# Performance work log

Hardware: AMD Instinct MI355X
Metric: run time of the kernel (lower is better)

The kernel has to match this reference:

```python
import jax, jax.numpy as jnp
import numpy as np

NUM_HEAD = 8
D_MODEL = 512
HEAD_DIM = D_MODEL // NUM_HEAD
SCALING = HEAD_DIM ** (-0.5)
B, NQ, NK = 2, 2048, 2048


def setup_inputs() -> dict:
    key = jax.random.key(0)
    ks = jax.random.split(key, 12)
    s = 1.0 / np.sqrt(D_MODEL)
    return {
        "q": jax.random.normal(ks[0], (B, NQ, D_MODEL), jnp.float32),
        "k": jax.random.normal(ks[1], (B, NK, D_MODEL), jnp.float32),
        "v": jax.random.normal(ks[2], (B, NK, D_MODEL), jnp.float32),
        "mask_head": jax.random.uniform(ks[3], (B, NUM_HEAD, NQ, NK), jnp.float32),
        "pearson_matrix": jax.random.normal(ks[4], (B, NUM_HEAD, NK, NK), jnp.float32),
        "Wq": jax.random.uniform(ks[5], (D_MODEL, D_MODEL), jnp.float32, -s, s),
        "bq": jax.random.uniform(ks[6], (D_MODEL,), jnp.float32, -s, s),
        "Wk": jax.random.uniform(ks[7], (D_MODEL, D_MODEL), jnp.float32, -s, s),
        "bk": jax.random.uniform(ks[8], (D_MODEL,), jnp.float32, -s, s),
        "Wv": jax.random.uniform(ks[9], (D_MODEL, D_MODEL), jnp.float32, -s, s),
        "bv": jax.random.uniform(ks[10], (D_MODEL,), jnp.float32, -s, s),
    }


def _split_heads(x):
    b, n, _ = x.shape
    return x.reshape(b, n, NUM_HEAD, HEAD_DIM).transpose(0, 2, 1, 3)  # b h n d


def reference(q, k, v, mask_head, pearson_matrix, Wq, bq, Wk, bk, Wv, bv):
    queries = _split_heads(q @ Wq.T + bq)
    keys = _split_heads(k @ Wk.T + bk)
    values = _split_heads(v @ Wv.T + bv)
    energy = jnp.einsum('bhqd,bhkd->bhqk', queries, keys) * SCALING
    att = jax.nn.softmax(energy, axis=-1)
    att = att * mask_head
    # einsum 'bhqk,bhkk->bhqk' = multiply by diagonal of pearson over last two axes
    diag = jnp.diagonal(pearson_matrix, axis1=-2, axis2=-1)  # b h k
    att = att * diag[:, :, None, :]
    agg = jnp.einsum('bhqk,bhkd->bhqd', att, values)
    b, h, n, d = agg.shape
    return agg.transpose(0, 2, 1, 3).reshape(b, n, h * d)
```

## Files before the change

kernel.cpp:

```cpp
#include <hip/hip_runtime.h>

#define NUM_HEAD 8
#define D_MODEL  512
#define HEAD_DIM 64
#define NSEQ     2048
#define SCALE_LOG2E 0.18033688011112042f

typedef __attribute__((ext_vector_type(8))) short bf16x8;
typedef __attribute__((ext_vector_type(4))) float f32x4;

static __device__ __forceinline__ unsigned short f2bf(float f) {
    unsigned u = __builtin_bit_cast(unsigned, f);
    u += 0x7fffu + ((u >> 16) & 1u);
    return (unsigned short)(u >> 16);
}
static __device__ __forceinline__ float bf2f(unsigned short h) {
    unsigned u = ((unsigned)h) << 16;
    return __builtin_bit_cast(float, u);
}
static __device__ __forceinline__ unsigned pk2(float a, float b) {
    return (unsigned)f2bf(a) | ((unsigned)f2bf(b) << 16);
}

#define PSTR 40

__global__ __launch_bounds__(256) void proj_kernel(
    const float* __restrict__ X, const float* __restrict__ W,
    const float* __restrict__ bias, unsigned short* __restrict__ outp)
{
    __shared__ unsigned short lA[128 * PSTR];
    __shared__ unsigned short lB[64 * PSTR];

    const int tid  = threadIdx.x;
    const int lane = tid & 63, wid = tid >> 6;
    const int quad = lane >> 4, l15 = lane & 15;
    const int wm = (wid >> 1) * 64;
    const int wn = (wid & 1) * 32;
    const int m0 = blockIdx.x * 128, n0 = blockIdx.y * 64;

    f32x4 acc[4][2];
    const f32x4 zf = {0.f, 0.f, 0.f, 0.f};
#pragma unroll
    for (int mi = 0; mi < 4; mi++)
#pragma unroll
        for (int ni = 0; ni < 2; ni++) acc[mi][ni] = zf;

    const int arow = tid >> 1, akc = (tid & 1) * 16;
    const int brow = tid >> 2, bkc = (tid & 3) * 8;

    for (int k0 = 0; k0 < D_MODEL; k0 += 32) {
        const float* ap = X + (m0 + arow) * D_MODEL + k0 + akc;
        float4 a0 = *(const float4*)(ap);
        float4 a1 = *(const float4*)(ap + 4);
        float4 a2 = *(const float4*)(ap + 8);
        float4 a3 = *(const float4*)(ap + 12);
        uint4 w0, w1;
        w0.x = pk2(a0.x, a0.y); w0.y = pk2(a0.z, a0.w);
        w0.z = pk2(a1.x, a1.y); w0.w = pk2(a1.z, a1.w);
        w1.x = pk2(a2.x, a2.y); w1.y = pk2(a2.z, a2.w);
        w1.z = pk2(a3.x, a3.y); w1.w = pk2(a3.z, a3.w);
        *(uint4*)&lA[arow * PSTR + akc]     = w0;
        *(uint4*)&lA[arow * PSTR + akc + 8] = w1;
        const float* bp = W + (n0 + brow) * D_MODEL + k0 + bkc;
        float4 b0 = *(const float4*)(bp);
        float4 b1 = *(const float4*)(bp + 4);
        uint4 wb;
        wb.x = pk2(b0.x, b0.y); wb.y = pk2(b0.z, b0.w);
        wb.z = pk2(b1.x, b1.y); wb.w = pk2(b1.z, b1.w);
        *(uint4*)&lB[brow * PSTR + bkc] = wb;
        __syncthreads();

        bf16x8 aF[4], bF[2];
#pragma unroll
        for (int mi = 0; mi < 4; mi++)
            aF[mi] = *(const bf16x8*)&lA[(wm + mi * 16 + l15) * PSTR + quad * 8];
#pragma unroll
        for (int ni = 0; ni < 2; ni++)
            bF[ni] = *(const bf16x8*)&lB[(wn + ni * 16 + l15) * PSTR + quad * 8];
#pragma unroll
        for (int mi = 0; mi < 4; mi++)
#pragma unroll
            for (int ni = 0; ni < 2; ni++)
                acc[mi][ni] = __builtin_amdgcn_mfma_f32_16x16x32_bf16(
                    aF[mi], bF[ni], acc[mi][ni], 0, 0, 0);
        __syncthreads();
    }

    const float bv0 = bias[n0 + wn + l15];
    const float bv1 = bias[n0 + wn + 16 + l15];
#pragma unroll
    for (int mi = 0; mi < 4; mi++) {
        const int mbase = m0 + wm + mi * 16 + quad * 4;
#pragma unroll
        for (int ni = 0; ni < 2; ni++) {
            const int c = n0 + wn + ni * 16 + l15;
            const int h = c >> 6, d = c & 63;
            const float bb_add = ni ? bv1 : bv0;
#pragma unroll
            for (int r = 0; r < 4; r++) {
                const int mm = mbase + r;
                const int bb = mm >> 11, n = mm & 2047;
                const float val = acc[mi][ni][r] + bb_add;
                outp[((bb * NUM_HEAD + h) * NSEQ + n) * HEAD_DIM + d] = f2bf(val);
            }
        }
    }
}

__global__ void diag_kernel(const float* __restrict__ pearson,
                            float* __restrict__ diag)
{
    const int t = blockIdx.x * blockDim.x + threadIdx.x;
    const int bh = t >> 11, kk = t & 2047;
    diag[t] = pearson[((size_t)(bh * NSEQ + kk)) * NSEQ + kk];
}

#define VSTR 72

__global__ __launch_bounds__(256) void attn_kernel(
    const unsigned short* __restrict__ Qp, const unsigned short* __restrict__ Kp,
    const unsigned short* __restrict__ Vp, const float* __restrict__ diag,
    const float* __restrict__ mask, float* __restrict__ out)
{
    __shared__ unsigned short lVt[64 * VSTR];
    __shared__ unsigned short lP[64 * VSTR];

    const int tid  = threadIdx.x;
    const int lane = tid & 63, wid = tid >> 6;
    const int quad = lane >> 4, l15 = lane & 15;
    const int bh = blockIdx.y;
    const int q0 = blockIdx.x * 64;

    const unsigned short* Qb = Qp + (size_t)bh * NSEQ * HEAD_DIM;
    const unsigned short* Kb = Kp + (size_t)bh * NSEQ * HEAD_DIM;
    const unsigned short* Vb = Vp + (size_t)bh * NSEQ * HEAD_DIM;
    const float* maskb = mask + (size_t)bh * NSEQ * NSEQ + (size_t)q0 * NSEQ;
    const float* diagb = diag + bh * NSEQ;

    bf16x8 qF[2];
    {
        const unsigned short* qp = Qb + (q0 + wid * 16 + l15) * HEAD_DIM + quad * 8;
        qF[0] = *(const bf16x8*)qp;
        qF[1] = *(const bf16x8*)(qp + 32);
    }

    const f32x4 zf = {0.f, 0.f, 0.f, 0.f};
    f32x4 oacc[4] = {zf, zf, zf, zf};
    float lacc[4] = {0.f, 0.f, 0.f, 0.f};

    const int vrow = tid >> 2;
    const int vdb  = (tid & 3) * 16;

    for (int kt = 0; kt < NSEQ; kt += 64) {
        bf16x8 kF[4][2];
#pragma unroll
        for (int nt = 0; nt < 4; nt++) {
            const unsigned short* kp = Kb + (kt + nt * 16 + l15) * HEAD_DIM + quad * 8;
            kF[nt][0] = *(const bf16x8*)kp;
            kF[nt][1] = *(const bf16x8*)(kp + 32);
        }
        float mv[4][4];
#pragma unroll
        for (int cf = 0; cf < 4; cf++)
#pragma unroll
            for (int r = 0; r < 4; r++)
                mv[cf][r] = maskb[(size_t)(wid * 16 + quad * 4 + r) * NSEQ + kt + cf * 16 + l15];

        {
            const float dg = diagb[kt + vrow];
            const unsigned short* vp = Vb + (kt + vrow) * HEAD_DIM + vdb;
            union { uint4 u; unsigned short s[8]; } va, vb2;
            va.u  = *(const uint4*)vp;
            vb2.u = *(const uint4*)(vp + 8);
#pragma unroll
            for (int i = 0; i < 8; i++) {
                lVt[(vdb + i) * VSTR + vrow]     = f2bf(bf2f(va.s[i]) * dg);
                lVt[(vdb + 8 + i) * VSTR + vrow] = f2bf(bf2f(vb2.s[i]) * dg);
            }
        }

        f32x4 sacc[4];
#pragma unroll
        for (int nt = 0; nt < 4; nt++) {
            sacc[nt] = __builtin_amdgcn_mfma_f32_16x16x32_bf16(qF[0], kF[nt][0], zf, 0, 0, 0);
            sacc[nt] = __builtin_amdgcn_mfma_f32_16x16x32_bf16(qF[1], kF[nt][1], sacc[nt], 0, 0, 0);
        }

#pragma unroll
        for (int cf = 0; cf < 4; cf++) {
#pragma unroll
            for (int r = 0; r < 4; r++) {
                const float p = __builtin_amdgcn_exp2f(sacc[cf][r] * SCALE_LOG2E);
                lacc[r] += p;
                lP[(wid * 16 + quad * 4 + r) * VSTR + cf * 16 + l15] = f2bf(p * mv[cf][r]);
            }
        }
        __syncthreads();

#pragma unroll
        for (int ks = 0; ks < 2; ks++) {
            const bf16x8 aP = *(const bf16x8*)&lP[(wid * 16 + l15) * VSTR + ks * 32 + quad * 8];
#pragma unroll
            for (int nt = 0; nt < 4; nt++) {
                const bf16x8 bV = *(const bf16x8*)&lVt[(nt * 16 + l15) * VSTR + ks * 32 + quad * 8];
                oacc[nt] = __builtin_amdgcn_mfma_f32_16x16x32_bf16(aP, bV, oacc[nt], 0, 0, 0);
            }
        }
        __syncthreads();
    }

#pragma unroll
    for (int r = 0; r < 4; r++) {
        float v = lacc[r];
        v += __shfl_xor(v, 1);
        v += __shfl_xor(v, 2);
        v += __shfl_xor(v, 4);
        v += __shfl_xor(v, 8);
        lacc[r] = v;
    }

    const int b = bh >> 3, h = bh & 7;
#pragma unroll
    for (int nt = 0; nt < 4; nt++)
#pragma unroll
        for (int r = 0; r < 4; r++) {
            const int qrow = q0 + wid * 16 + quad * 4 + r;
            out[((size_t)b * NSEQ + qrow) * D_MODEL + h * HEAD_DIM + nt * 16 + l15] =
                oacc[nt][r] / lacc[r];
        }
}

extern "C" void kernel_launch(void* const* d_in, const int* in_sizes, int n_in,
                              void* d_out, int out_size, void* d_ws, size_t ws_size,
                              hipStream_t stream) {
    const float* q       = (const float*)d_in[0];
    const float* k       = (const float*)d_in[1];
    const float* v       = (const float*)d_in[2];
    const float* mask    = (const float*)d_in[3];
    const float* pearson = (const float*)d_in[4];
    const float* Wq      = (const float*)d_in[5];
    const float* bq      = (const float*)d_in[6];
    const float* Wk      = (const float*)d_in[7];
    const float* bk      = (const float*)d_in[8];
    const float* Wv      = (const float*)d_in[9];
    const float* bv      = (const float*)d_in[10];

    unsigned short* Qp = (unsigned short*)d_ws;
    unsigned short* Kp = Qp + 2097152;
    unsigned short* Vp = Kp + 2097152;
    float* diag = (float*)((char*)d_ws + 12582912);
    float* out = (float*)d_out;

    proj_kernel<<<dim3(32, 8), 256, 0, stream>>>(q, Wq, bq, Qp);
    proj_kernel<<<dim3(32, 8), 256, 0, stream>>>(k, Wk, bk, Kp);
    proj_kernel<<<dim3(32, 8), 256, 0, stream>>>(v, Wv, bv, Vp);
    diag_kernel<<<dim3(128), 256, 0, stream>>>(pearson, diag);
    attn_kernel<<<dim3(32, 16), 256, 0, stream>>>(Qp, Kp, Vp, diag, mask, out);
}
```

Measured before the change: 589.9 us.

## Pre-transpose V, fold diag into P, register double-buffer K/mask tiles

The projection kernel now runs Q, K and V in a single launch using blockIdx.z, and writes V transposed (head_dim x seq) with packed 4-wide stores. The attention kernel reads V fragments straight from global memory, so the LDS transpose of V and both block-wide __syncthreads are gone; each wave keeps a private P buffer. The pearson diagonal is applied to P instead of V. K, mask and diag for the next tile are prefetched into registers (ping-pong) while the current tile is computed. In exchange, register pressure rises and V is re-read from global/L2 by every wave.

```diff
diff --git a/kernel.cpp b/kernel.cpp
--- a/kernel.cpp
+++ b/kernel.cpp
@@ -25,11 +25,20 @@
 #define PSTR 40
 
 __global__ __launch_bounds__(256) void proj_kernel(
-    const float* __restrict__ X, const float* __restrict__ W,
-    const float* __restrict__ bias, unsigned short* __restrict__ outp)
+    const float* __restrict__ Xq, const float* __restrict__ Xk, const float* __restrict__ Xv,
+    const float* __restrict__ Wq, const float* __restrict__ Wk, const float* __restrict__ Wv,
+    const float* __restrict__ Bq, const float* __restrict__ Bk, const float* __restrict__ Bv,
+    unsigned short* __restrict__ Oq, unsigned short* __restrict__ Ok,
+    unsigned short* __restrict__ Ov)
 {
     __shared__ unsigned short lA[128 * PSTR];
     __shared__ unsigned short lB[64 * PSTR];
+
+    const int z = blockIdx.z;
+    const float* X    = (z == 0) ? Xq : (z == 1) ? Xk : Xv;
+    const float* W    = (z == 0) ? Wq : (z == 1) ? Wk : Wv;
+    const float* bias = (z == 0) ? Bq : (z == 1) ? Bk : Bv;
+    unsigned short* outp = (z == 0) ? Oq : (z == 1) ? Ok : Ov;
 
     const int tid  = threadIdx.x;
     const int lane = tid & 63, wid = tid >> 6;
@@ -88,20 +97,41 @@
 
     const float bv0 = bias[n0 + wn + l15];
     const float bv1 = bias[n0 + wn + 16 + l15];
-#pragma unroll
-    for (int mi = 0; mi < 4; mi++) {
-        const int mbase = m0 + wm + mi * 16 + quad * 4;
-#pragma unroll
-        for (int ni = 0; ni < 2; ni++) {
-            const int c = n0 + wn + ni * 16 + l15;
-            const int h = c >> 6, d = c & 63;
-            const float bb_add = ni ? bv1 : bv0;
-#pragma unroll
-            for (int r = 0; r < 4; r++) {
-                const int mm = mbase + r;
-                const int bb = mm >> 11, n = mm & 2047;
-                const float val = acc[mi][ni][r] + bb_add;
-                outp[((bb * NUM_HEAD + h) * NSEQ + n) * HEAD_DIM + d] = f2bf(val);
+
+    if (z == 2) {
+#pragma unroll
+        for (int mi = 0; mi < 4; mi++) {
+            const int mbase = m0 + wm + mi * 16 + quad * 4;
+            const int bb = mbase >> 11, n = mbase & 2047;
+#pragma unroll
+            for (int ni = 0; ni < 2; ni++) {
+                const int c = n0 + wn + ni * 16 + l15;
+                const int h = c >> 6, d = c & 63;
+                const float badd = ni ? bv1 : bv0;
+                ushort4 pk;
+                pk.x = f2bf(acc[mi][ni][0] + badd);
+                pk.y = f2bf(acc[mi][ni][1] + badd);
+                pk.z = f2bf(acc[mi][ni][2] + badd);
+                pk.w = f2bf(acc[mi][ni][3] + badd);
+                *(ushort4*)&outp[((size_t)((bb * NUM_HEAD + h) * HEAD_DIM + d)) * NSEQ + n] = pk;
+            }
+        }
+    } else {
+#pragma unroll
+        for (int mi = 0; mi < 4; mi++) {
+            const int mbase = m0 + wm + mi * 16 + quad * 4;
+#pragma unroll
+            for (int ni = 0; ni < 2; ni++) {
+                const int c = n0 + wn + ni * 16 + l15;
+                const int h = c >> 6, d = c & 63;
+                const float badd = ni ? bv1 : bv0;
+#pragma unroll
+                for (int r = 0; r < 4; r++) {
+                    const int mm = mbase + r;
+                    const int bb = mm >> 11, n = mm & 2047;
+                    outp[((bb * NUM_HEAD + h) * NSEQ + n) * HEAD_DIM + d] =
+                        f2bf(acc[mi][ni][r] + badd);
+                }
             }
         }
     }
@@ -117,29 +147,34 @@
 
 #define VSTR 72
 
+struct TileRegs {
+    bf16x8 kF[4][2];
+    float  mv[4][4];
+    float  dg[4];
+};
+
 __global__ __launch_bounds__(256) void attn_kernel(
     const unsigned short* __restrict__ Qp, const unsigned short* __restrict__ Kp,
-    const unsigned short* __restrict__ Vp, const float* __restrict__ diag,
+    const unsigned short* __restrict__ Vt, const float* __restrict__ diag,
     const float* __restrict__ mask, float* __restrict__ out)
 {
-    __shared__ unsigned short lVt[64 * VSTR];
-    __shared__ unsigned short lP[64 * VSTR];
+    __shared__ unsigned short lP[4][16 * VSTR];
 
     const int tid  = threadIdx.x;
     const int lane = tid & 63, wid = tid >> 6;
     const int quad = lane >> 4, l15 = lane & 15;
     const int bh = blockIdx.y;
-    const int q0 = blockIdx.x * 64;
+    const int q0 = blockIdx.x * 64 + wid * 16;
 
     const unsigned short* Qb = Qp + (size_t)bh * NSEQ * HEAD_DIM;
     const unsigned short* Kb = Kp + (size_t)bh * NSEQ * HEAD_DIM;
-    const unsigned short* Vb = Vp + (size_t)bh * NSEQ * HEAD_DIM;
-    const float* maskb = mask + (size_t)bh * NSEQ * NSEQ + (size_t)q0 * NSEQ;
+    const unsigned short* Vb = Vt + (size_t)bh * HEAD_DIM * NSEQ;
     const float* diagb = diag + bh * NSEQ;
+    const float* mrow  = mask + (size_t)bh * NSEQ * NSEQ + (size_t)(q0 + quad * 4) * NSEQ;
 
     bf16x8 qF[2];
     {
-        const unsigned short* qp = Qb + (q0 + wid * 16 + l15) * HEAD_DIM + quad * 8;
+        const unsigned short* qp = Qb + (q0 + l15) * HEAD_DIM + quad * 8;
         qF[0] = *(const bf16x8*)qp;
         qF[1] = *(const bf16x8*)(qp + 32);
     }
@@ -148,42 +183,38 @@
     f32x4 oacc[4] = {zf, zf, zf, zf};
     float lacc[4] = {0.f, 0.f, 0.f, 0.f};
 
-    const int vrow = tid >> 2;
-    const int vdb  = (tid & 3) * 16;
-
-    for (int kt = 0; kt < NSEQ; kt += 64) {
-        bf16x8 kF[4][2];
+    unsigned short* lPw = &lP[wid][0];
+
+    auto load_tile = [&](TileRegs& t, int ktt) {
 #pragma unroll
         for (int nt = 0; nt < 4; nt++) {
-            const unsigned short* kp = Kb + (kt + nt * 16 + l15) * HEAD_DIM + quad * 8;
-            kF[nt][0] = *(const bf16x8*)kp;
-            kF[nt][1] = *(const bf16x8*)(kp + 32);
-        }
-        float mv[4][4];
-#pragma unroll
-        for (int cf = 0; cf < 4; cf++)
+            const unsigned short* kp = Kb + (ktt + nt * 16 + l15) * HEAD_DIM + quad * 8;
+            t.kF[nt][0] = *(const bf16x8*)kp;
+            t.kF[nt][1] = *(const bf16x8*)(kp + 32);
+        }
+#pragma unroll
+        for (int cf = 0; cf < 4; cf++) {
+            t.dg[cf] = diagb[ktt + cf * 16 + l15];
 #pragma unroll
             for (int r = 0; r < 4; r++)
-                mv[cf][r] = maskb[(size_t)(wid * 16 + quad * 4 + r) * NSEQ + kt + cf * 16 + l15];
-
-        {
-            const float dg = diagb[kt + vrow];
-            const unsigned short* vp = Vb + (kt + vrow) * HEAD_DIM + vdb;
-            union { uint4 u; unsigned short s[8]; } va, vb2;
-            va.u  = *(const uint4*)vp;
-            vb2.u = *(const uint4*)(vp + 8);
-#pragma unroll
-            for (int i = 0; i < 8; i++) {
-                lVt[(vdb + i) * VSTR + vrow]     = f2bf(bf2f(va.s[i]) * dg);
-                lVt[(vdb + 8 + i) * VSTR + vrow] = f2bf(bf2f(vb2.s[i]) * dg);
-            }
+                t.mv[cf][r] = mrow[(size_t)r * NSEQ + ktt + cf * 16 + l15];
+        }
+    };
+
+    auto compute_tile = [&](const TileRegs& t, int ktt) {
+        bf16x8 vF[4][2];
+#pragma unroll
+        for (int nt = 0; nt < 4; nt++) {
+            const unsigned short* vp = Vb + (nt * 16 + l15) * NSEQ + ktt + quad * 8;
+            vF[nt][0] = *(const bf16x8*)vp;
+            vF[nt][1] = *(const bf16x8*)(vp + 32);
         }
 
         f32x4 sacc[4];
 #pragma unroll
         for (int nt = 0; nt < 4; nt++) {
-            sacc[nt] = __builtin_amdgcn_mfma_f32_16x16x32_bf16(qF[0], kF[nt][0], zf, 0, 0, 0);
-            sacc[nt] = __builtin_amdgcn_mfma_f32_16x16x32_bf16(qF[1], kF[nt][1], sacc[nt], 0, 0, 0);
+            sacc[nt] = __builtin_amdgcn_mfma_f32_16x16x32_bf16(qF[0], t.kF[nt][0], zf, 0, 0, 0);
+            sacc[nt] = __builtin_amdgcn_mfma_f32_16x16x32_bf16(qF[1], t.kF[nt][1], sacc[nt], 0, 0, 0);
         }
 
 #pragma unroll
@@ -192,21 +223,28 @@
             for (int r = 0; r < 4; r++) {
                 const float p = __builtin_amdgcn_exp2f(sacc[cf][r] * SCALE_LOG2E);
                 lacc[r] += p;
-                lP[(wid * 16 + quad * 4 + r) * VSTR + cf * 16 + l15] = f2bf(p * mv[cf][r]);
+                lPw[(quad * 4 + r) * VSTR + cf * 16 + l15] =
+                    f2bf(p * t.mv[cf][r] * t.dg[cf]);
             }
         }
-        __syncthreads();
 
 #pragma unroll
         for (int ks = 0; ks < 2; ks++) {
-            const bf16x8 aP = *(const bf16x8*)&lP[(wid * 16 + l15) * VSTR + ks * 32 + quad * 8];
-#pragma unroll
-            for (int nt = 0; nt < 4; nt++) {
-                const bf16x8 bV = *(const bf16x8*)&lVt[(nt * 16 + l15) * VSTR + ks * 32 + quad * 8];
-                oacc[nt] = __builtin_amdgcn_mfma_f32_16x16x32_bf16(aP, bV, oacc[nt], 0, 0, 0);
-            }
-        }
-        __syncthreads();
+            const bf16x8 aP = *(const bf16x8*)&lPw[l15 * VSTR + ks * 32 + quad * 8];
+#pragma unroll
+            for (int nt = 0; nt < 4; nt++)
+                oacc[nt] = __builtin_amdgcn_mfma_f32_16x16x32_bf16(aP, vF[nt][ks], oacc[nt], 0, 0, 0);
+        }
+    };
+
+    TileRegs tA, tB;
+    load_tile(tA, 0);
+    for (int kt = 0; kt < NSEQ; kt += 128) {
+        load_tile(tB, kt + 64);
+        compute_tile(tA, kt);
+        const int ktn = (kt + 128 < NSEQ) ? (kt + 128) : (NSEQ - 64);
+        load_tile(tA, ktn);
+        compute_tile(tB, kt + 64);
     }
 
 #pragma unroll
@@ -224,7 +262,7 @@
     for (int nt = 0; nt < 4; nt++)
 #pragma unroll
         for (int r = 0; r < 4; r++) {
-            const int qrow = q0 + wid * 16 + quad * 4 + r;
+            const int qrow = q0 + quad * 4 + r;
             out[((size_t)b * NSEQ + qrow) * D_MODEL + h * HEAD_DIM + nt * 16 + l15] =
                 oacc[nt][r] / lacc[r];
         }
@@ -247,13 +285,12 @@
 
     unsigned short* Qp = (unsigned short*)d_ws;
     unsigned short* Kp = Qp + 2097152;
-    unsigned short* Vp = Kp + 2097152;
+    unsigned short* Vt = Kp + 2097152;
     float* diag = (float*)((char*)d_ws + 12582912);
     float* out = (float*)d_out;
 
-    proj_kernel<<<dim3(32, 8), 256, 0, stream>>>(q, Wq, bq, Qp);
-    proj_kernel<<<dim3(32, 8), 256, 0, stream>>>(k, Wk, bk, Kp);
-    proj_kernel<<<dim3(32, 8), 256, 0, stream>>>(v, Wv, bv, Vp);
+    proj_kernel<<<dim3(32, 8, 3), 256, 0, stream>>>(q, k, v, Wq, Wk, Wv,
+                                                    bq, bk, bv, Qp, Kp, Vt);
     diag_kernel<<<dim3(128), 256, 0, stream>>>(pearson, diag);
-    attn_kernel<<<dim3(32, 16), 256, 0, stream>>>(Qp, Kp, Vp, diag, mask, out);
-}
+    attn_kernel<<<dim3(32, 16), 256, 0, stream>>>(Qp, Kp, Vt, diag, mask, out);
+}
```

New measurement: 571.5 us. 3.1% less time.
